# Performance work log

Measured on AMD Instinct MI355X. Metric: run time of the kernel, lower is better.

## Reference

```python
import jax, jax.numpy as jnp
import numpy as np

TEMPERATURE = 0.04
LAMBDA_KOLEO = 0.1
EPS_NORM = 1e-12
EPS_KOLEO = 1e-9


def setup_inputs() -> dict:
    key = jax.random.key(0)
    k1, k2 = jax.random.split(key)
    N, D = 8192, 512
    z1 = jax.random.normal(k1, (N, D), dtype=jnp.float32)
    z2 = jax.random.normal(k2, (N, D), dtype=jnp.float32)
    return {"z1": z1, "z2": z2}


def _l2_normalize(x):
    # matches F.normalize(x, dim=1) with default eps=1e-12
    n = jnp.linalg.norm(x, axis=1, keepdims=True)
    return x / jnp.maximum(n, EPS_NORM)


def _infonce(queries, keys, temperature):
    # [N, N] similarity logits; labels are the diagonal
    logits = (queries @ keys.T) / temperature
    logp = jax.nn.log_softmax(logits, axis=1)
    return -jnp.mean(jnp.diagonal(logp))


def _koleo(emb):
    # pairwise euclidean distances via gram trick (matches torch.cdist p=2)
    sq = jnp.sum(emb * emb, axis=1)
    d2 = sq[:, None] + sq[None, :] - 2.0 * (emb @ emb.T)
    d = jnp.sqrt(jnp.maximum(d2, 0.0))
    N = emb.shape[0]
    eye = jnp.eye(N, dtype=bool)
    d = jnp.where(eye, jnp.inf, d)
    min_d = jnp.min(d, axis=1)
    return -jnp.mean(jnp.log(min_d + EPS_KOLEO))


def reference(z1, z2):
    z1 = _l2_normalize(z1)
    z2 = _l2_normalize(z2)
    loss_12 = _infonce(z1, z2, TEMPERATURE)
    loss_21 = _infonce(z2, z1, TEMPERATURE)
    loss_contrastive = (loss_12 + loss_21) / 2
    koleo_1 = _koleo(z1)
    koleo_2 = _koleo(z2)
    loss_koleo = (koleo_1 + koleo_2) / 2
    total_loss = loss_contrastive + LAMBDA_KOLEO * loss_koleo
    return total_loss
```

## Files before the change

### kernel.cpp

```cpp
#include <hip/hip_runtime.h>
#include <hip/hip_bf16.h>
#include <hip/hip_fp8.h>
#include <math.h>

#define N 8192
#define D 512
#define BM 128
#define BK 64
#define NSTRIP 64
#define S_BLOCKS (NSTRIP * NSTRIP)
#define TRI (NSTRIP * (NSTRIP + 1) / 2)
#define G_BLOCKS (2 * TRI)

typedef float f32x4 __attribute__((ext_vector_type(4)));
typedef long l2 __attribute__((ext_vector_type(2)));

__device__ inline void gload_lds16(const void* g, void* l) {
  __builtin_amdgcn_global_load_lds(
      (const __attribute__((address_space(1))) void*)g,
      (__attribute__((address_space(3))) void*)l, 16, 0, 0);
}

__global__ __launch_bounds__(256) void norm_kernel(
    const float* __restrict__ z1, const float* __restrict__ z2,
    unsigned char* __restrict__ q1, unsigned char* __restrict__ q2,
    float* __restrict__ diag) {
  int row = blockIdx.x;
  int t = threadIdx.x;
  const float* a = z1 + (size_t)row * D;
  const float* b = z2 + (size_t)row * D;
  float va[2], vb[2];
  float ss1 = 0.f, ss2 = 0.f, dd = 0.f;
#pragma unroll
  for (int i = 0; i < 2; i++) {
    float x = a[t + 256 * i];
    float y = b[t + 256 * i];
    va[i] = x; vb[i] = y;
    ss1 += x * x; ss2 += y * y; dd += x * y;
  }
#pragma unroll
  for (int off = 1; off < 64; off <<= 1) {
    ss1 += __shfl_xor(ss1, off);
    ss2 += __shfl_xor(ss2, off);
    dd  += __shfl_xor(dd,  off);
  }
  __shared__ float red[3][4];
  int wv = t >> 6;
  if ((t & 63) == 0) { red[0][wv] = ss1; red[1][wv] = ss2; red[2][wv] = dd; }
  __syncthreads();
  ss1 = red[0][0] + red[0][1] + red[0][2] + red[0][3];
  ss2 = red[1][0] + red[1][1] + red[1][2] + red[1][3];
  dd  = red[2][0] + red[2][1] + red[2][2] + red[2][3];
  float i1 = 1.0f / fmaxf(sqrtf(ss1), 1e-12f);
  float i2 = 1.0f / fmaxf(sqrtf(ss2), 1e-12f);
#pragma unroll
  for (int i = 0; i < 2; i++) {
    __hip_fp8_e4m3 c1((float)(va[i] * i1));
    __hip_fp8_e4m3 c2((float)(vb[i] * i2));
    q1[(size_t)row * D + t + 256 * i] = c1.__x;
    q2[(size_t)row * D + t + 256 * i] = c2.__x;
  }
  if (t == 0) diag[row] = dd * i1 * i2;
}

__device__ __forceinline__ void mm_tile_fp8(
    const unsigned char* __restrict__ X, const unsigned char* __restrict__ Y,
    int r0, int c0, unsigned char* At, unsigned char* Bt, f32x4 (&acc)[4][4],
    int t, int lr, int quad, int rw, int cw) {
  const f32x4 vzero = {0.0f, 0.0f, 0.0f, 0.0f};
#pragma unroll
  for (int i = 0; i < 4; i++)
#pragma unroll
    for (int j = 0; j < 4; j++) acc[i][j] = vzero;

  for (int kc = 0; kc < 8; kc++) {
    int k0 = kc * BK;
    __syncthreads();
#pragma unroll
    for (int it = 0; it < 2; it++) {
      int s = it * 256 + t;
      int row = s >> 2, cs = s & 3;
      int src = cs ^ ((row >> 1) & 3);
      gload_lds16(X + (size_t)(r0 + row) * D + k0 + src * 16, &At[s * 16]);
    }
#pragma unroll
    for (int it = 0; it < 2; it++) {
      int s = it * 256 + t;
      int row = s >> 2, cs = s & 3;
      int src = cs ^ ((row >> 1) & 3);
      gload_lds16(Y + (size_t)(c0 + row) * D + k0 + src * 16, &Bt[s * 16]);
    }
    __syncthreads();

    l2 af[4], bf[4];
#pragma unroll
    for (int i = 0; i < 4; i++) {
      int row = rw * 64 + i * 16 + lr;
      int ps = quad ^ ((row >> 1) & 3);
      af[i] = *(const l2*)&At[row * 64 + ps * 16];
    }
#pragma unroll
    for (int j = 0; j < 4; j++) {
      int row = cw * 64 + j * 16 + lr;
      int ps = quad ^ ((row >> 1) & 3);
      bf[j] = *(const l2*)&Bt[row * 64 + ps * 16];
    }
#pragma unroll
    for (int i = 0; i < 4; i++)
#pragma unroll
      for (int j = 0; j < 4; j++)
        acc[i][j] = __builtin_amdgcn_mfma_f32_16x16x32_fp8_fp8(af[i].x, bf[j].x, acc[i][j], 0, 0, 0);
#pragma unroll
    for (int i = 0; i < 4; i++)
#pragma unroll
      for (int j = 0; j < 4; j++)
        acc[i][j] = __builtin_amdgcn_mfma_f32_16x16x32_fp8_fp8(af[i].y, bf[j].y, acc[i][j], 0, 0, 0);
  }
}

__global__ __launch_bounds__(256, 4) void s_kernel(
    const unsigned char* __restrict__ q1, const unsigned char* __restrict__ q2,
    float* __restrict__ rowS, float* __restrict__ colS) {
  __shared__ unsigned char At[BM * BK];
  __shared__ unsigned char Bt[BM * BK];
  __shared__ float redA[2][BM];
  __shared__ float redC[2][BM];

  int bx = blockIdx.x;
  int t = threadIdx.x;
  int lane = t & 63;
  int wave = t >> 6;
  int quad = lane >> 4;
  int lr = lane & 15;
  int rw = wave >> 1;
  int cw = wave & 1;
  const float scale = 1.4426950408889634f / 0.04f;

  int strip = bx >> 6;
  int ct = bx & 63;
  int r0 = strip * BM;
  int c0 = ct * BM;

  f32x4 acc[4][4];
  mm_tile_fp8(q1, q2, r0, c0, At, Bt, acc, t, lr, quad, rw, cw);

  float rowacc[4][4];
  float colacc[4] = {0.0f, 0.0f, 0.0f, 0.0f};
#pragma unroll
  for (int i = 0; i < 4; i++)
#pragma unroll
    for (int r = 0; r < 4; r++) rowacc[i][r] = 0.0f;
#pragma unroll
  for (int i = 0; i < 4; i++)
#pragma unroll
    for (int j = 0; j < 4; j++)
#pragma unroll
      for (int r = 0; r < 4; r++) {
        float e = __builtin_amdgcn_exp2f(acc[i][j][r] * scale);
        rowacc[i][r] += e;
        colacc[j] += e;
      }
#pragma unroll
  for (int j = 0; j < 4; j++) {
    colacc[j] += __shfl_xor(colacc[j], 16);
    colacc[j] += __shfl_xor(colacc[j], 32);
  }
  if (lane < 16) {
#pragma unroll
    for (int j = 0; j < 4; j++) redA[rw][cw * 64 + j * 16 + lr] = colacc[j];
  }
  __syncthreads();
  if (t < BM) colS[(size_t)strip * N + c0 + t] = redA[0][t] + redA[1][t];

#pragma unroll
  for (int i = 0; i < 4; i++)
#pragma unroll
    for (int r = 0; r < 4; r++) {
      float v = rowacc[i][r];
#pragma unroll
      for (int off = 1; off < 16; off <<= 1) v += __shfl_xor(v, off);
      if (lr == 0) redC[cw][rw * 64 + i * 16 + quad * 4 + r] = v;
    }
  __syncthreads();
  if (t < BM) rowS[(size_t)ct * N + r0 + t] = redC[0][t] + redC[1][t];
}

__global__ __launch_bounds__(256, 4) void g_kernel(
    const unsigned char* __restrict__ q1, const unsigned char* __restrict__ q2,
    float* __restrict__ partG) {
  __shared__ unsigned char At[BM * BK];
  __shared__ unsigned char Bt[BM * BK];
  __shared__ float redA[2][BM];
  __shared__ float redB[2][BM];

  int bx = blockIdx.x;
  int t = threadIdx.x;
  int lane = t & 63;
  int wave = t >> 6;
  int quad = lane >> 4;
  int lr = lane & 15;
  int rw = wave >> 1;
  int cw = wave & 1;

  int g = (bx >= TRI) ? 1 : 0;
  int tri = bx - g * TRI;
  int a = (int)((sqrtf(8.0f * (float)tri + 1.0f) - 1.0f) * 0.5f);
  while ((a + 1) * (a + 2) / 2 <= tri) a++;
  while (a * (a + 1) / 2 > tri) a--;
  int b = tri - a * (a + 1) / 2;
  const unsigned char* X = g ? q2 : q1;
  int r0 = a * BM;
  int c0 = b * BM;
  bool diagb = (a == b);

  f32x4 acc[4][4];
  mm_tile_fp8(X, X, r0, c0, At, Bt, acc, t, lr, quad, rw, cw);

#pragma unroll
  for (int i = 0; i < 4; i++)
#pragma unroll
    for (int r = 0; r < 4; r++) {
      int rr = rw * 64 + i * 16 + quad * 4 + r;
      float v = -3.0e38f;
#pragma unroll
      for (int j = 0; j < 4; j++) {
        float x = acc[i][j][r];
        int cc = cw * 64 + j * 16 + lr;
        if (diagb && cc == rr) x = -3.0e38f;
        v = fmaxf(v, x);
      }
#pragma unroll
      for (int off = 1; off < 16; off <<= 1) v = fmaxf(v, __shfl_xor(v, off));
      if (lr == 0) redA[cw][rr] = v;
    }
  __syncthreads();
  if (t < BM)
    partG[((size_t)(g * NSTRIP + b)) * N + r0 + t] = fmaxf(redA[0][t], redA[1][t]);

  if (!diagb) {
#pragma unroll
    for (int j = 0; j < 4; j++) {
      float m = acc[0][j][0];
#pragma unroll
      for (int i = 0; i < 4; i++)
#pragma unroll
        for (int r = 0; r < 4; r++) m = fmaxf(m, acc[i][j][r]);
      m = fmaxf(m, __shfl_xor(m, 16));
      m = fmaxf(m, __shfl_xor(m, 32));
      if (lane < 16) redB[rw][cw * 64 + j * 16 + lr] = m;
    }
    __syncthreads();
    if (t < BM)
      partG[((size_t)(g * NSTRIP + a)) * N + c0 + t] = fmaxf(redB[0][t], redB[1][t]);
  }
}

__global__ __launch_bounds__(256) void combine_kernel(
    const float* __restrict__ diag,
    const float* __restrict__ rowS, const float* __restrict__ colS,
    const float* __restrict__ partG, float* __restrict__ bp) {
  const float invT = 25.0f;
  int i = blockIdx.x * 256 + threadIdx.x;

  float s = 0.0f;
  for (int q = 0; q < NSTRIP; q++) s += rowS[(size_t)q * N + i];
  float a12 = logf(s) - diag[i] * invT;

  s = 0.0f;
  for (int o = 0; o < NSTRIP; o++) s += colS[(size_t)o * N + i];
  float a21 = logf(s) - diag[i] * invT;

  float g1 = -3.0e38f, g2 = -3.0e38f;
  for (int o = 0; o < NSTRIP; o++) {
    g1 = fmaxf(g1, partG[(size_t)o * N + i]);
    g2 = fmaxf(g2, partG[(size_t)(NSTRIP + o) * N + i]);
  }
  float k1 = logf(sqrtf(fmaxf(2.0f - 2.0f * g1, 0.0f)) + 1e-9f);
  float k2 = logf(sqrtf(fmaxf(2.0f - 2.0f * g2, 0.0f)) + 1e-9f);

#pragma unroll
  for (int off = 1; off < 64; off <<= 1) {
    a12 += __shfl_xor(a12, off);
    a21 += __shfl_xor(a21, off);
    k1  += __shfl_xor(k1,  off);
    k2  += __shfl_xor(k2,  off);
  }
  __shared__ float fr[4][4];
  int wv = threadIdx.x >> 6;
  if ((threadIdx.x & 63) == 0) { fr[0][wv] = a12; fr[1][wv] = a21; fr[2][wv] = k1; fr[3][wv] = k2; }
  __syncthreads();
  if (threadIdx.x == 0) {
    bp[blockIdx.x * 4 + 0] = fr[0][0] + fr[0][1] + fr[0][2] + fr[0][3];
    bp[blockIdx.x * 4 + 1] = fr[1][0] + fr[1][1] + fr[1][2] + fr[1][3];
    bp[blockIdx.x * 4 + 2] = fr[2][0] + fr[2][1] + fr[2][2] + fr[2][3];
    bp[blockIdx.x * 4 + 3] = fr[3][0] + fr[3][1] + fr[3][2] + fr[3][3];
  }
}

__global__ __launch_bounds__(64) void final_kernel(const float* __restrict__ bp,
                                                   float* __restrict__ out) {
  int t = threadIdx.x;
  float a12 = 0.f, a21 = 0.f, k1 = 0.f, k2 = 0.f;
  if (t < 32) {
    a12 = bp[t * 4 + 0];
    a21 = bp[t * 4 + 1];
    k1  = bp[t * 4 + 2];
    k2  = bp[t * 4 + 3];
  }
#pragma unroll
  for (int off = 1; off < 64; off <<= 1) {
    a12 += __shfl_xor(a12, off);
    a21 += __shfl_xor(a21, off);
    k1  += __shfl_xor(k1,  off);
    k2  += __shfl_xor(k2,  off);
  }
  if (t == 0) {
    float contrastive = 0.5f * (a12 + a21) / (float)N;
    float koleo = -0.5f * (k1 + k2) / (float)N;
    out[0] = contrastive + 0.1f * koleo;
  }
}

extern "C" void kernel_launch(void* const* d_in, const int* in_sizes, int n_in,
                              void* d_out, int out_size, void* d_ws, size_t ws_size,
                              hipStream_t stream) {
  const float* z1 = (const float*)d_in[0];
  const float* z2 = (const float*)d_in[1];
  char* w = (char*)d_ws;
  unsigned char* q1 = (unsigned char*)w; w += (size_t)N * D;
  unsigned char* q2 = (unsigned char*)w; w += (size_t)N * D;
  float* diag = (float*)w;   w += (size_t)N * sizeof(float);
  float* rowS = (float*)w;   w += (size_t)NSTRIP * N * sizeof(float);
  float* colS = (float*)w;   w += (size_t)NSTRIP * N * sizeof(float);
  float* partG = (float*)w;  w += (size_t)2 * NSTRIP * N * sizeof(float);
  float* bp = (float*)w;     w += (size_t)32 * 4 * sizeof(float);
  float* out = (float*)d_out;

  norm_kernel<<<N, 256, 0, stream>>>(z1, z2, q1, q2, diag);
  s_kernel<<<S_BLOCKS, 256, 0, stream>>>(q1, q2, rowS, colS);
  g_kernel<<<G_BLOCKS, 256, 0, stream>>>(q1, q2, partG);
  combine_kernel<<<N / 256, 256, 0, stream>>>(diag, rowS, colS, partG, bp);
  final_kernel<<<1, 64, 0, stream>>>(bp, out);
}
```

Baseline: 200.0 us.

## Switch fp8 GEMM to 16x16x128 scaled MFMA with 128-wide K tiles

Replaces the pair of 16x16x32 fp8 MFMAs per K=64 step with the gfx950 16x16x128 f8f6f4 scaled MFMA (unit scales) and doubles the K tile to 128 bytes, halving the number of K iterations and syncs. The LDS swizzle is reworked for 8 16-byte chunks per row, and each fragment is now built from two 16-byte LDS reads. LDS per block doubles, so launch bounds drop to 3 blocks per CU, which may reduce occupancy and latency hiding.

```diff
diff --git a/kernel.cpp b/kernel.cpp
--- a/kernel.cpp
+++ b/kernel.cpp
@@ -6,14 +6,15 @@
 #define N 8192
 #define D 512
 #define BM 128
-#define BK 64
+#define BKB 128
 #define NSTRIP 64
 #define S_BLOCKS (NSTRIP * NSTRIP)
 #define TRI (NSTRIP * (NSTRIP + 1) / 2)
 #define G_BLOCKS (2 * TRI)
 
 typedef float f32x4 __attribute__((ext_vector_type(4)));
-typedef long l2 __attribute__((ext_vector_type(2)));
+typedef int i32x4 __attribute__((ext_vector_type(4)));
+typedef int i32x8 __attribute__((ext_vector_type(8)));
 
 __device__ inline void gload_lds16(const void* g, void* l) {
   __builtin_amdgcn_global_load_lds(
@@ -73,56 +74,56 @@
 #pragma unroll
     for (int j = 0; j < 4; j++) acc[i][j] = vzero;
 
-  for (int kc = 0; kc < 8; kc++) {
-    int k0 = kc * BK;
+  for (int kc = 0; kc < 4; kc++) {
+    int k0 = kc * BKB;
     __syncthreads();
 #pragma unroll
-    for (int it = 0; it < 2; it++) {
+    for (int it = 0; it < 4; it++) {
       int s = it * 256 + t;
-      int row = s >> 2, cs = s & 3;
-      int src = cs ^ ((row >> 1) & 3);
+      int row = s >> 3, cs = s & 7;
+      int src = cs ^ (row & 7);
       gload_lds16(X + (size_t)(r0 + row) * D + k0 + src * 16, &At[s * 16]);
     }
 #pragma unroll
-    for (int it = 0; it < 2; it++) {
+    for (int it = 0; it < 4; it++) {
       int s = it * 256 + t;
-      int row = s >> 2, cs = s & 3;
-      int src = cs ^ ((row >> 1) & 3);
+      int row = s >> 3, cs = s & 7;
+      int src = cs ^ (row & 7);
       gload_lds16(Y + (size_t)(c0 + row) * D + k0 + src * 16, &Bt[s * 16]);
     }
     __syncthreads();
 
-    l2 af[4], bf[4];
+    i32x8 af[4], bf[4];
 #pragma unroll
     for (int i = 0; i < 4; i++) {
       int row = rw * 64 + i * 16 + lr;
-      int ps = quad ^ ((row >> 1) & 3);
-      af[i] = *(const l2*)&At[row * 64 + ps * 16];
+      int ps0 = (2 * quad) ^ (row & 7);
+      i32x4 lo = *(const i32x4*)&At[row * BKB + ps0 * 16];
+      i32x4 hi = *(const i32x4*)&At[row * BKB + (ps0 ^ 1) * 16];
+      af[i] = __builtin_shufflevector(lo, hi, 0, 1, 2, 3, 4, 5, 6, 7);
     }
 #pragma unroll
     for (int j = 0; j < 4; j++) {
       int row = cw * 64 + j * 16 + lr;
-      int ps = quad ^ ((row >> 1) & 3);
-      bf[j] = *(const l2*)&Bt[row * 64 + ps * 16];
+      int ps0 = (2 * quad) ^ (row & 7);
+      i32x4 lo = *(const i32x4*)&Bt[row * BKB + ps0 * 16];
+      i32x4 hi = *(const i32x4*)&Bt[row * BKB + (ps0 ^ 1) * 16];
+      bf[j] = __builtin_shufflevector(lo, hi, 0, 1, 2, 3, 4, 5, 6, 7);
     }
 #pragma unroll
     for (int i = 0; i < 4; i++)
 #pragma unroll
       for (int j = 0; j < 4; j++)
-        acc[i][j] = __builtin_amdgcn_mfma_f32_16x16x32_fp8_fp8(af[i].x, bf[j].x, acc[i][j], 0, 0, 0);
-#pragma unroll
-    for (int i = 0; i < 4; i++)
-#pragma unroll
-      for (int j = 0; j < 4; j++)
-        acc[i][j] = __builtin_amdgcn_mfma_f32_16x16x32_fp8_fp8(af[i].y, bf[j].y, acc[i][j], 0, 0, 0);
-  }
-}
-
-__global__ __launch_bounds__(256, 4) void s_kernel(
+        acc[i][j] = __builtin_amdgcn_mfma_scale_f32_16x16x128_f8f6f4(
+            af[i], bf[j], acc[i][j], 0, 0, 0, 127, 0, 127);
+  }
+}
+
+__global__ __launch_bounds__(256, 3) void s_kernel(
     const unsigned char* __restrict__ q1, const unsigned char* __restrict__ q2,
     float* __restrict__ rowS, float* __restrict__ colS) {
-  __shared__ unsigned char At[BM * BK];
-  __shared__ unsigned char Bt[BM * BK];
+  __shared__ unsigned char At[BM * BKB];
+  __shared__ unsigned char Bt[BM * BKB];
   __shared__ float redA[2][BM];
   __shared__ float redC[2][BM];
 
@@ -185,11 +186,11 @@
   if (t < BM) rowS[(size_t)ct * N + r0 + t] = redC[0][t] + redC[1][t];
 }
 
-__global__ __launch_bounds__(256, 4) void g_kernel(
+__global__ __launch_bounds__(256, 3) void g_kernel(
     const unsigned char* __restrict__ q1, const unsigned char* __restrict__ q2,
     float* __restrict__ partG) {
-  __shared__ unsigned char At[BM * BK];
-  __shared__ unsigned char Bt[BM * BK];
+  __shared__ unsigned char At[BM * BKB];
+  __shared__ unsigned char Bt[BM * BKB];
   __shared__ float redA[2][BM];
   __shared__ float redB[2][BM];
 
```

Result: slower. 400.0 us (+100.0%).

## Merge similarity and koleo GEMM kernels and fold final reduction into atomics

Applied to the files above, without the earlier changes.

The separate InfoNCE logsumexp GEMM kernel and the koleo max-similarity GEMM kernel become one launch that picks its mode from the block index. The combine step now scales each per-block partial and atomically adds it into the output, which norm_kernel zeroes first, so final_kernel is removed. This cuts two launches and the tail gaps between the GEMM grids. In exchange, launch bounds drop from 4 to 3 waves per SIMD to cover the larger merged body, which may reduce occupancy, and float atomics make the summation order nondeterministic.

```diff
diff --git a/kernel.cpp b/kernel.cpp
--- a/kernel.cpp
+++ b/kernel.cpp
@@ -11,6 +11,7 @@
 #define S_BLOCKS (NSTRIP * NSTRIP)
 #define TRI (NSTRIP * (NSTRIP + 1) / 2)
 #define G_BLOCKS (2 * TRI)
+#define SG_BLOCKS (S_BLOCKS + G_BLOCKS)
 
 typedef float f32x4 __attribute__((ext_vector_type(4)));
 typedef long l2 __attribute__((ext_vector_type(2)));
@@ -24,9 +25,10 @@
 __global__ __launch_bounds__(256) void norm_kernel(
     const float* __restrict__ z1, const float* __restrict__ z2,
     unsigned char* __restrict__ q1, unsigned char* __restrict__ q2,
-    float* __restrict__ diag) {
+    float* __restrict__ diag, float* __restrict__ out) {
   int row = blockIdx.x;
   int t = threadIdx.x;
+  if (row == 0 && t == 0) out[0] = 0.0f;
   const float* a = z1 + (size_t)row * D;
   const float* b = z2 + (size_t)row * D;
   float va[2], vb[2];
@@ -118,13 +120,14 @@
   }
 }
 
-__global__ __launch_bounds__(256, 4) void s_kernel(
+__global__ __launch_bounds__(256, 3) void sg_kernel(
     const unsigned char* __restrict__ q1, const unsigned char* __restrict__ q2,
-    float* __restrict__ rowS, float* __restrict__ colS) {
+    float* __restrict__ rowS, float* __restrict__ colS,
+    float* __restrict__ partG) {
   __shared__ unsigned char At[BM * BK];
   __shared__ unsigned char Bt[BM * BK];
   __shared__ float redA[2][BM];
-  __shared__ float redC[2][BM];
+  __shared__ float redB[2][BM];
 
   int bx = blockIdx.x;
   int t = threadIdx.x;
@@ -136,129 +139,118 @@
   int cw = wave & 1;
   const float scale = 1.4426950408889634f / 0.04f;
 
-  int strip = bx >> 6;
-  int ct = bx & 63;
-  int r0 = strip * BM;
-  int c0 = ct * BM;
+  bool smode = bx < S_BLOCKS;
+  const unsigned char* X;
+  const unsigned char* Y;
+  int r0, c0, ga = 0, gb = 0, gg = 0;
+  bool diagb = false;
+  if (smode) {
+    r0 = (bx >> 6) * BM;
+    c0 = (bx & 63) * BM;
+    X = q1; Y = q2;
+  } else {
+    int gx = bx - S_BLOCKS;
+    gg = (gx >= TRI) ? 1 : 0;
+    int tri = gx - gg * TRI;
+    int a = (int)((sqrtf(8.0f * (float)tri + 1.0f) - 1.0f) * 0.5f);
+    while ((a + 1) * (a + 2) / 2 <= tri) a++;
+    while (a * (a + 1) / 2 > tri) a--;
+    int b = tri - a * (a + 1) / 2;
+    ga = a; gb = b;
+    X = gg ? q2 : q1; Y = X;
+    r0 = a * BM;
+    c0 = b * BM;
+    diagb = (a == b);
+  }
 
   f32x4 acc[4][4];
-  mm_tile_fp8(q1, q2, r0, c0, At, Bt, acc, t, lr, quad, rw, cw);
-
-  float rowacc[4][4];
-  float colacc[4] = {0.0f, 0.0f, 0.0f, 0.0f};
-#pragma unroll
-  for (int i = 0; i < 4; i++)
-#pragma unroll
-    for (int r = 0; r < 4; r++) rowacc[i][r] = 0.0f;
-#pragma unroll
-  for (int i = 0; i < 4; i++)
-#pragma unroll
-    for (int j = 0; j < 4; j++)
+  mm_tile_fp8(X, Y, r0, c0, At, Bt, acc, t, lr, quad, rw, cw);
+
+  if (smode) {
+    float rowacc[4][4];
+    float colacc[4] = {0.0f, 0.0f, 0.0f, 0.0f};
+#pragma unroll
+    for (int i = 0; i < 4; i++)
+#pragma unroll
+      for (int r = 0; r < 4; r++) rowacc[i][r] = 0.0f;
+#pragma unroll
+    for (int i = 0; i < 4; i++)
+#pragma unroll
+      for (int j = 0; j < 4; j++)
+#pragma unroll
+        for (int r = 0; r < 4; r++) {
+          float e = __builtin_amdgcn_exp2f(acc[i][j][r] * scale);
+          rowacc[i][r] += e;
+          colacc[j] += e;
+        }
+#pragma unroll
+    for (int j = 0; j < 4; j++) {
+      colacc[j] += __shfl_xor(colacc[j], 16);
+      colacc[j] += __shfl_xor(colacc[j], 32);
+    }
+    if (lane < 16) {
+#pragma unroll
+      for (int j = 0; j < 4; j++) redA[rw][cw * 64 + j * 16 + lr] = colacc[j];
+    }
+    __syncthreads();
+    if (t < BM) colS[(size_t)(r0 >> 7) * N + c0 + t] = redA[0][t] + redA[1][t];
+
+#pragma unroll
+    for (int i = 0; i < 4; i++)
 #pragma unroll
       for (int r = 0; r < 4; r++) {
-        float e = __builtin_amdgcn_exp2f(acc[i][j][r] * scale);
-        rowacc[i][r] += e;
-        colacc[j] += e;
+        float v = rowacc[i][r];
+#pragma unroll
+        for (int off = 1; off < 16; off <<= 1) v += __shfl_xor(v, off);
+        if (lr == 0) redB[cw][rw * 64 + i * 16 + quad * 4 + r] = v;
       }
-#pragma unroll
-  for (int j = 0; j < 4; j++) {
-    colacc[j] += __shfl_xor(colacc[j], 16);
-    colacc[j] += __shfl_xor(colacc[j], 32);
-  }
-  if (lane < 16) {
-#pragma unroll
-    for (int j = 0; j < 4; j++) redA[rw][cw * 64 + j * 16 + lr] = colacc[j];
-  }
-  __syncthreads();
-  if (t < BM) colS[(size_t)strip * N + c0 + t] = redA[0][t] + redA[1][t];
-
-#pragma unroll
-  for (int i = 0; i < 4; i++)
-#pragma unroll
-    for (int r = 0; r < 4; r++) {
-      float v = rowacc[i][r];
-#pragma unroll
-      for (int off = 1; off < 16; off <<= 1) v += __shfl_xor(v, off);
-      if (lr == 0) redC[cw][rw * 64 + i * 16 + quad * 4 + r] = v;
-    }
-  __syncthreads();
-  if (t < BM) rowS[(size_t)ct * N + r0 + t] = redC[0][t] + redC[1][t];
-}
-
-__global__ __launch_bounds__(256, 4) void g_kernel(
-    const unsigned char* __restrict__ q1, const unsigned char* __restrict__ q2,
-    float* __restrict__ partG) {
-  __shared__ unsigned char At[BM * BK];
-  __shared__ unsigned char Bt[BM * BK];
-  __shared__ float redA[2][BM];
-  __shared__ float redB[2][BM];
-
-  int bx = blockIdx.x;
-  int t = threadIdx.x;
-  int lane = t & 63;
-  int wave = t >> 6;
-  int quad = lane >> 4;
-  int lr = lane & 15;
-  int rw = wave >> 1;
-  int cw = wave & 1;
-
-  int g = (bx >= TRI) ? 1 : 0;
-  int tri = bx - g * TRI;
-  int a = (int)((sqrtf(8.0f * (float)tri + 1.0f) - 1.0f) * 0.5f);
-  while ((a + 1) * (a + 2) / 2 <= tri) a++;
-  while (a * (a + 1) / 2 > tri) a--;
-  int b = tri - a * (a + 1) / 2;
-  const unsigned char* X = g ? q2 : q1;
-  int r0 = a * BM;
-  int c0 = b * BM;
-  bool diagb = (a == b);
-
-  f32x4 acc[4][4];
-  mm_tile_fp8(X, X, r0, c0, At, Bt, acc, t, lr, quad, rw, cw);
-
-#pragma unroll
-  for (int i = 0; i < 4; i++)
-#pragma unroll
-    for (int r = 0; r < 4; r++) {
-      int rr = rw * 64 + i * 16 + quad * 4 + r;
-      float v = -3.0e38f;
+    __syncthreads();
+    if (t < BM) rowS[(size_t)(c0 >> 7) * N + r0 + t] = redB[0][t] + redB[1][t];
+  } else {
+#pragma unroll
+    for (int i = 0; i < 4; i++)
+#pragma unroll
+      for (int r = 0; r < 4; r++) {
+        int rr = rw * 64 + i * 16 + quad * 4 + r;
+        float v = -3.0e38f;
+#pragma unroll
+        for (int j = 0; j < 4; j++) {
+          float x = acc[i][j][r];
+          int cc = cw * 64 + j * 16 + lr;
+          if (diagb && cc == rr) x = -3.0e38f;
+          v = fmaxf(v, x);
+        }
+#pragma unroll
+        for (int off = 1; off < 16; off <<= 1) v = fmaxf(v, __shfl_xor(v, off));
+        if (lr == 0) redA[cw][rr] = v;
+      }
+    __syncthreads();
+    if (t < BM)
+      partG[((size_t)(gg * NSTRIP + gb)) * N + r0 + t] = fmaxf(redA[0][t], redA[1][t]);
+
+    if (!diagb) {
 #pragma unroll
       for (int j = 0; j < 4; j++) {
-        float x = acc[i][j][r];
-        int cc = cw * 64 + j * 16 + lr;
-        if (diagb && cc == rr) x = -3.0e38f;
-        v = fmaxf(v, x);
+        float m = acc[0][j][0];
+#pragma unroll
+        for (int i = 0; i < 4; i++)
+#pragma unroll
+          for (int r = 0; r < 4; r++) m = fmaxf(m, acc[i][j][r]);
+        m = fmaxf(m, __shfl_xor(m, 16));
+        m = fmaxf(m, __shfl_xor(m, 32));
+        if (lane < 16) redB[rw][cw * 64 + j * 16 + lr] = m;
       }
-#pragma unroll
-      for (int off = 1; off < 16; off <<= 1) v = fmaxf(v, __shfl_xor(v, off));
-      if (lr == 0) redA[cw][rr] = v;
-    }
-  __syncthreads();
-  if (t < BM)
-    partG[((size_t)(g * NSTRIP + b)) * N + r0 + t] = fmaxf(redA[0][t], redA[1][t]);
-
-  if (!diagb) {
-#pragma unroll
-    for (int j = 0; j < 4; j++) {
-      float m = acc[0][j][0];
-#pragma unroll
-      for (int i = 0; i < 4; i++)
-#pragma unroll
-        for (int r = 0; r < 4; r++) m = fmaxf(m, acc[i][j][r]);
-      m = fmaxf(m, __shfl_xor(m, 16));
-      m = fmaxf(m, __shfl_xor(m, 32));
-      if (lane < 16) redB[rw][cw * 64 + j * 16 + lr] = m;
-    }
-    __syncthreads();
-    if (t < BM)
-      partG[((size_t)(g * NSTRIP + a)) * N + c0 + t] = fmaxf(redB[0][t], redB[1][t]);
+      __syncthreads();
+      if (t < BM)
+        partG[((size_t)(gg * NSTRIP + ga)) * N + c0 + t] = fmaxf(redB[0][t], redB[1][t]);
+    }
   }
 }
 
 __global__ __launch_bounds__(256) void combine_kernel(
     const float* __restrict__ diag,
     const float* __restrict__ rowS, const float* __restrict__ colS,
-    const float* __restrict__ partG, float* __restrict__ bp) {
+    const float* __restrict__ partG, float* __restrict__ out) {
   const float invT = 25.0f;
   int i = blockIdx.x * 256 + threadIdx.x;
 
@@ -278,47 +270,15 @@
   float k1 = logf(sqrtf(fmaxf(2.0f - 2.0f * g1, 0.0f)) + 1e-9f);
   float k2 = logf(sqrtf(fmaxf(2.0f - 2.0f * g2, 0.0f)) + 1e-9f);
 
-#pragma unroll
-  for (int off = 1; off < 64; off <<= 1) {
-    a12 += __shfl_xor(a12, off);
-    a21 += __shfl_xor(a21, off);
-    k1  += __shfl_xor(k1,  off);
-    k2  += __shfl_xor(k2,  off);
-  }
-  __shared__ float fr[4][4];
+  float c = 0.5f * (a12 + a21) / (float)N - 0.1f * 0.5f * (k1 + k2) / (float)N;
+#pragma unroll
+  for (int off = 1; off < 64; off <<= 1) c += __shfl_xor(c, off);
+  __shared__ float fr[4];
   int wv = threadIdx.x >> 6;
-  if ((threadIdx.x & 63) == 0) { fr[0][wv] = a12; fr[1][wv] = a21; fr[2][wv] = k1; fr[3][wv] = k2; }
+  if ((threadIdx.x & 63) == 0) fr[wv] = c;
   __syncthreads();
-  if (threadIdx.x == 0) {
-    bp[blockIdx.x * 4 + 0] = fr[0][0] + fr[0][1] + fr[0][2] + fr[0][3];
-    bp[blockIdx.x * 4 + 1] = fr[1][0] + fr[1][1] + fr[1][2] + fr[1][3];
-    bp[blockIdx.x * 4 + 2] = fr[2][0] + fr[2][1] + fr[2][2] + fr[2][3];
-    bp[blockIdx.x * 4 + 3] = fr[3][0] + fr[3][1] + fr[3][2] + fr[3][3];
-  }
-}
-
-__global__ __launch_bounds__(64) void final_kernel(const float* __restrict__ bp,
-                                                   float* __restrict__ out) {
-  int t = threadIdx.x;
-  float a12 = 0.f, a21 = 0.f, k1 = 0.f, k2 = 0.f;
-  if (t < 32) {
-    a12 = bp[t * 4 + 0];
-    a21 = bp[t * 4 + 1];
-    k1  = bp[t * 4 + 2];
-    k2  = bp[t * 4 + 3];
-  }
-#pragma unroll
-  for (int off = 1; off < 64; off <<= 1) {
-    a12 += __shfl_xor(a12, off);
-    a21 += __shfl_xor(a21, off);
-    k1  += __shfl_xor(k1,  off);
-    k2  += __shfl_xor(k2,  off);
-  }
-  if (t == 0) {
-    float contrastive = 0.5f * (a12 + a21) / (float)N;
-    float koleo = -0.5f * (k1 + k2) / (float)N;
-    out[0] = contrastive + 0.1f * koleo;
-  }
+  if (threadIdx.x == 0)
+    atomicAdd(out, fr[0] + fr[1] + fr[2] + fr[3]);
 }
 
 extern "C" void kernel_launch(void* const* d_in, const int* in_sizes, int n_in,
@@ -333,12 +293,9 @@
   float* rowS = (float*)w;   w += (size_t)NSTRIP * N * sizeof(float);
   float* colS = (float*)w;   w += (size_t)NSTRIP * N * sizeof(float);
   float* partG = (float*)w;  w += (size_t)2 * NSTRIP * N * sizeof(float);
-  float* bp = (float*)w;     w += (size_t)32 * 4 * sizeof(float);
   float* out = (float*)d_out;
 
-  norm_kernel<<<N, 256, 0, stream>>>(z1, z2, q1, q2, diag);
-  s_kernel<<<S_BLOCKS, 256, 0, stream>>>(q1, q2, rowS, colS);
-  g_kernel<<<G_BLOCKS, 256, 0, stream>>>(q1, q2, partG);
-  combine_kernel<<<N / 256, 256, 0, stream>>>(diag, rowS, colS, partG, bp);
-  final_kernel<<<1, 64, 0, stream>>>(bp, out);
-}
+  norm_kernel<<<N, 256, 0, stream>>>(z1, z2, q1, q2, diag, out);
+  sg_kernel<<<SG_BLOCKS, 256, 0, stream>>>(q1, q2, rowS, colS, partG);
+  combine_kernel<<<N / 256, 256, 0, stream>>>(diag, rowS, colS, partG, out);
+}
```

Result: faster. 190.7 us (-4.6%).
